# Kernel tuning notes

Hardware: AMD Instinct MI355X
Metric: run time of the kernel (lower is better)

Reference implementation:

```python
import jax, jax.numpy as jnp
import numpy as np

R = 16
ALPHA = 32.0
SCALING = ALPHA / R


def setup_inputs() -> dict:
    key = jax.random.key(0)
    ks = jax.random.split(key, 6)
    B, T, C, O, E = 16, 1500, 1024, 1024, 8
    x = jax.random.normal(ks[0], (B, T, C), dtype=jnp.float32)
    # gate weights per batch element (e.g. softmax-like, but module accepts any)
    w = jax.random.uniform(ks[1], (B, E), dtype=jnp.float32)
    W_base = jax.random.normal(ks[2], (O, C), dtype=jnp.float32) * 0.02
    b_base = jax.random.normal(ks[3], (O,), dtype=jnp.float32) * 0.02
    As = jax.random.normal(ks[4], (E, R, C), dtype=jnp.float32) * 0.02
    Bs = jax.random.normal(ks[5], (E, O, R), dtype=jnp.float32) * 0.02
    return {"x": x, "w": w, "W_base": W_base, "b_base": b_base, "As": As, "Bs": Bs}


def reference(x, w, W_base, b_base, As, Bs):
    # base linear: (B,T,C) @ (C,O) + b
    out = jnp.einsum('btc,oc->bto', x, W_base) + b_base
    # per-expert low-rank: h[b,t,e,r] = x[b,t,:] @ A_e^T
    h = jnp.einsum('btc,erc->bter', x, As)          # (B,T,E,R)
    # y[b,t,e,o] = h @ B_e^T ; gate-weighted sum over experts
    lora = jnp.einsum('bter,eor,be->bto', h, Bs, w)  # (B,T,O)
    return out + lora * SCALING
```

## Files before the change

### kernel.cpp

```cpp
#include <hip/hip_runtime.h>
#include <stdint.h>
#include <stddef.h>


#define B_ 16
#define T_ 1500
#define C_ 1024
#define O_ 1024
#define E_ 8
#define R_ 16
#define ER 128
#define KK 1152
#define BT 24000
#define SCALING 2.0f

typedef __bf16 bf16x8 __attribute__((ext_vector_type(8)));
typedef float f32x4 __attribute__((ext_vector_type(4)));
typedef unsigned short u16;

__device__ inline u16 f2bf(float f) {
  union { float f; unsigned u; } v; v.f = f;
  unsigned u = v.u;
  u += 0x7fff + ((u >> 16) & 1);
  return (u16)(u >> 16);
}

#define GLL(gp, lp)                                                            \
  __builtin_amdgcn_global_load_lds(                                            \
      (const __attribute__((address_space(1))) void*)(gp),                     \
      (__attribute__((address_space(3))) void*)(lp), 16, 0, 0)

__global__ __launch_bounds__(256) void prep_w(const float* __restrict__ Wb,
                                              const float* __restrict__ Bs,
                                              const float* __restrict__ As,
                                              u16* __restrict__ wp,
                                              u16* __restrict__ ap) {
  int idx = blockIdx.x * 256 + threadIdx.x;
  if (idx < O_ * KK) {
    int o = idx / KK;
    int k = idx - o * KK;
    float v;
    if (k < C_) {
      v = Wb[o * C_ + k];
    } else {
      int j = k - C_;
      v = Bs[((j >> 4) * O_ + o) * R_ + (j & 15)];
    }
    wp[idx] = f2bf(v);
  } else {
    int a = idx - O_ * KK;
    ap[a] = f2bf(As[a]);
  }
}

__global__ __launch_bounds__(256) void cvt_h(const float* __restrict__ x,
                                             const u16* __restrict__ ab,
                                             const float* __restrict__ w,
                                             u16* __restrict__ xp) {
  const int mt = blockIdx.x;
  const int tid = threadIdx.x, lane = tid & 63, wv = tid >> 6;
  const int wrow = wv & 1, wcol = wv >> 1, l15 = lane & 15, quad = lane >> 4;
  const int s7 = l15 & 7;

  __shared__ u16 lA[32 * 72];
  __shared__ u16 lB[128 * 64];

  const size_t row0 = (size_t)mt * 32;

  f32x4 acc[4];
#pragma unroll
  for (int j = 0; j < 4; ++j) acc[j] = (f32x4){0.f, 0.f, 0.f, 0.f};

  int brow[4], bko[4];
#pragma unroll
  for (int c = 0; c < 4; ++c) {
    int idx = c * 256 + tid;
    brow[c] = idx >> 3;
    bko[c] = (((idx & 7) ^ (brow[c] & 7)) << 3);
  }

  const int xr = tid >> 3;
  const int xc = (tid & 7) * 4;

  for (int kt = 0; kt < C_ / 64; ++kt) {
    const int k0 = kt * 64;
#pragma unroll
    for (int c = 0; c < 4; ++c)
      GLL(ab + brow[c] * C_ + k0 + bko[c], &lB[(c * 256 + tid) * 8]);
    float4 v0 = *(const float4*)&x[(row0 + xr) * C_ + k0 + xc];
    float4 v1 = *(const float4*)&x[(row0 + xr) * C_ + k0 + 32 + xc];
    ushort4 o0, o1;
    o0.x = f2bf(v0.x); o0.y = f2bf(v0.y); o0.z = f2bf(v0.z); o0.w = f2bf(v0.w);
    o1.x = f2bf(v1.x); o1.y = f2bf(v1.y); o1.z = f2bf(v1.z); o1.w = f2bf(v1.w);
    *(ushort4*)&lA[xr * 72 + xc] = o0;
    *(ushort4*)&lA[xr * 72 + 32 + xc] = o1;
    *(ushort4*)&xp[(row0 + xr) * KK + k0 + xc] = o0;
    *(ushort4*)&xp[(row0 + xr) * KK + k0 + 32 + xc] = o1;
    __syncthreads();
#pragma unroll
    for (int kk = 0; kk < 2; ++kk) {
      bf16x8 af = *(const bf16x8*)&lA[(wrow * 16 + l15) * 72 + kk * 32 + quad * 8];
      bf16x8 bfr[4];
#pragma unroll
      for (int j = 0; j < 4; ++j)
        bfr[j] = *(const bf16x8*)&lB[(wcol * 64 + j * 16 + l15) * 64 +
                                     (((kk * 4 + quad) ^ s7) << 3)];
#pragma unroll
      for (int j = 0; j < 4; ++j)
        acc[j] = __builtin_amdgcn_mfma_f32_16x16x32_bf16(af, bfr[j], acc[j], 0, 0, 0);
    }
    __syncthreads();
  }

#pragma unroll
  for (int j = 0; j < 4; ++j) {
    const int col = wcol * 64 + j * 16 + l15;
    const int e = wcol * 4 + j;
#pragma unroll
    for (int rr = 0; rr < 4; ++rr) {
      const int row = mt * 32 + wrow * 16 + quad * 4 + rr;
      const int b = row / T_;
      xp[(size_t)row * KK + C_ + col] = f2bf(acc[j][rr] * (SCALING * w[b * E_ + e]));
    }
  }
}

__global__ __launch_bounds__(256) void main_gemm(const u16* __restrict__ xp,
                                                 const u16* __restrict__ wp,
                                                 const float* __restrict__ bb,
                                                 float* __restrict__ out) {
  const int id = blockIdx.x;
  const int mt = ((id >> 6) << 3) | (id & 7);
  const int nt = (id >> 3) & 7;
  if (mt >= 188) return;
  const int tid = threadIdx.x, lane = tid & 63, wv = tid >> 6;
  const int wrow = wv & 1, wcol = wv >> 1, l15 = lane & 15, quad = lane >> 4;
  const int s7 = l15 & 7;

  __shared__ u16 lA[128 * 64];
  __shared__ u16 lB[128 * 64];
  const u16* gA = xp + (size_t)mt * 128 * KK;
  const u16* gB = wp + (size_t)nt * 128 * KK;

  f32x4 acc[4][4];
#pragma unroll
  for (int i = 0; i < 4; ++i)
#pragma unroll
    for (int j = 0; j < 4; ++j) acc[i][j] = (f32x4){0.f, 0.f, 0.f, 0.f};

  int srow[4], sko[4];
#pragma unroll
  for (int c = 0; c < 4; ++c) {
    int idx = c * 256 + tid;
    srow[c] = idx >> 3;
    sko[c] = (((idx & 7) ^ (srow[c] & 7)) << 3);
  }

  for (int kt = 0; kt < KK / 64; ++kt) {
    const int k0 = kt * 64;
#pragma unroll
    for (int c = 0; c < 4; ++c)
      GLL(gA + (size_t)srow[c] * KK + k0 + sko[c], &lA[(c * 256 + tid) * 8]);
#pragma unroll
    for (int c = 0; c < 4; ++c)
      GLL(gB + (size_t)srow[c] * KK + k0 + sko[c], &lB[(c * 256 + tid) * 8]);
    __syncthreads();
#pragma unroll
    for (int kk = 0; kk < 2; ++kk) {
      bf16x8 af[4], bfr[4];
#pragma unroll
      for (int i = 0; i < 4; ++i) {
        const int ko = (((kk * 4 + quad) ^ s7) << 3);
        af[i] = *(const bf16x8*)&lA[(wrow * 64 + i * 16 + l15) * 64 + ko];
        bfr[i] = *(const bf16x8*)&lB[(wcol * 64 + i * 16 + l15) * 64 + ko];
      }
#pragma unroll
      for (int i = 0; i < 4; ++i)
#pragma unroll
        for (int j = 0; j < 4; ++j)
          acc[i][j] = __builtin_amdgcn_mfma_f32_16x16x32_bf16(af[i], bfr[j], acc[i][j], 0, 0, 0);
    }
    __syncthreads();
  }

#pragma unroll
  for (int j = 0; j < 4; ++j) {
    const int col = nt * 128 + wcol * 64 + j * 16 + l15;
    const float bias = bb[col];
#pragma unroll
    for (int i = 0; i < 4; ++i) {
#pragma unroll
      for (int rr = 0; rr < 4; ++rr) {
        const int row = mt * 128 + wrow * 64 + i * 16 + quad * 4 + rr;
        if (row < BT) out[(size_t)row * O_ + col] = acc[i][j][rr] + bias;
      }
    }
  }
}

extern "C" void kernel_launch(void* const* d_in, const int* in_sizes, int n_in,
                              void* d_out, int out_size, void* d_ws, size_t ws_size,
                              hipStream_t stream) {
  const float* x = (const float*)d_in[0];
  const float* w = (const float*)d_in[1];
  const float* Wb = (const float*)d_in[2];
  const float* bb = (const float*)d_in[3];
  const float* As = (const float*)d_in[4];
  const float* Bs = (const float*)d_in[5];
  float* out = (float*)d_out;

  u16* xp = (u16*)d_ws;
  u16* wp = xp + (size_t)BT * KK;
  u16* ap = wp + (size_t)O_ * KK;

  prep_w<<<(O_ * KK + ER * C_) / 256, 256, 0, stream>>>(Wb, Bs, As, wp, ap);
  cvt_h<<<750, 256, 0, stream>>>(x, ap, w, xp);
  main_gemm<<<1536, 256, 0, stream>>>(xp, wp, bb, out);
}
```

Before: 285.7 us.

## Double-buffer main GEMM LDS loads with 256x128 tiles and K-step 32

The main GEMM tile grows from 128x128 to 256x128 so each wave holds an 8x4 block of MFMA accumulators, and the K step drops from 64 to 32. LDS is double-buffered and the next tile's global_load_lds is issued before computing on the current one, with explicit waitcnt/barrier control and raised wave priority around the MFMA loop. This aims to overlap global-to-LDS traffic with matrix math and to raise arithmetic intensity per block. In exchange the XOR swizzle is dropped, which may cause LDS bank conflicts, register pressure rises under launch_bounds(256,2), and the grid is halved to 768 blocks (752 active), which increases tail imbalance.

```diff
diff --git a/kernel.cpp b/kernel.cpp
--- a/kernel.cpp
+++ b/kernel.cpp
@@ -12,6 +12,7 @@
 #define ER 128
 #define KK 1152
 #define BT 24000
+#define NT 36
 #define SCALING 2.0f
 
 typedef __bf16 bf16x8 __attribute__((ext_vector_type(8)));
@@ -125,73 +126,97 @@
   }
 }
 
-__global__ __launch_bounds__(256) void main_gemm(const u16* __restrict__ xp,
-                                                 const u16* __restrict__ wp,
-                                                 const float* __restrict__ bb,
-                                                 float* __restrict__ out) {
+__global__ __launch_bounds__(256, 2) void main_gemm(const u16* __restrict__ xp,
+                                                    const u16* __restrict__ wp,
+                                                    const float* __restrict__ bb,
+                                                    float* __restrict__ out) {
   const int id = blockIdx.x;
   const int mt = ((id >> 6) << 3) | (id & 7);
   const int nt = (id >> 3) & 7;
-  if (mt >= 188) return;
+  if (mt >= 94) return;
   const int tid = threadIdx.x, lane = tid & 63, wv = tid >> 6;
-  const int wrow = wv & 1, wcol = wv >> 1, l15 = lane & 15, quad = lane >> 4;
-  const int s7 = l15 & 7;
-
-  __shared__ u16 lA[128 * 64];
-  __shared__ u16 lB[128 * 64];
-  const u16* gA = xp + (size_t)mt * 128 * KK;
+  const int wm = wv >> 1, wn = wv & 1, l15 = lane & 15, quad = lane >> 4;
+
+  __shared__ u16 lA[2][256 * 32];
+  __shared__ u16 lB[2][128 * 32];
+
+  const u16* gA = xp + (size_t)mt * 256 * KK;
   const u16* gB = wp + (size_t)nt * 128 * KK;
 
-  f32x4 acc[4][4];
-#pragma unroll
-  for (int i = 0; i < 4; ++i)
+  f32x4 acc[8][4];
+#pragma unroll
+  for (int i = 0; i < 8; ++i)
 #pragma unroll
     for (int j = 0; j < 4; ++j) acc[i][j] = (f32x4){0.f, 0.f, 0.f, 0.f};
 
-  int srow[4], sko[4];
+  const u16* pa[4];
+  const u16* pb[2];
+  int dA[4], dB[2];
 #pragma unroll
   for (int c = 0; c < 4; ++c) {
     int idx = c * 256 + tid;
-    srow[c] = idx >> 3;
-    sko[c] = (((idx & 7) ^ (srow[c] & 7)) << 3);
-  }
-
-  for (int kt = 0; kt < KK / 64; ++kt) {
-    const int k0 = kt * 64;
-#pragma unroll
-    for (int c = 0; c < 4; ++c)
-      GLL(gA + (size_t)srow[c] * KK + k0 + sko[c], &lA[(c * 256 + tid) * 8]);
-#pragma unroll
-    for (int c = 0; c < 4; ++c)
-      GLL(gB + (size_t)srow[c] * KK + k0 + sko[c], &lB[(c * 256 + tid) * 8]);
-    __syncthreads();
-#pragma unroll
-    for (int kk = 0; kk < 2; ++kk) {
-      bf16x8 af[4], bfr[4];
-#pragma unroll
-      for (int i = 0; i < 4; ++i) {
-        const int ko = (((kk * 4 + quad) ^ s7) << 3);
-        af[i] = *(const bf16x8*)&lA[(wrow * 64 + i * 16 + l15) * 64 + ko];
-        bfr[i] = *(const bf16x8*)&lB[(wcol * 64 + i * 16 + l15) * 64 + ko];
-      }
-#pragma unroll
-      for (int i = 0; i < 4; ++i)
-#pragma unroll
-        for (int j = 0; j < 4; ++j)
-          acc[i][j] = __builtin_amdgcn_mfma_f32_16x16x32_bf16(af[i], bfr[j], acc[i][j], 0, 0, 0);
-    }
-    __syncthreads();
+    pa[c] = gA + (size_t)(idx >> 2) * KK + (idx & 3) * 8;
+    dA[c] = idx * 8;
+  }
+#pragma unroll
+  for (int c = 0; c < 2; ++c) {
+    int idx = c * 256 + tid;
+    pb[c] = gB + (size_t)(idx >> 2) * KK + (idx & 3) * 8;
+    dB[c] = idx * 8;
+  }
+
+  const int offA = (wm * 128 + l15) * 32 + quad * 8;
+  const int offB = (wn * 64 + l15) * 32 + quad * 8;
+
+#pragma unroll
+  for (int c = 0; c < 4; ++c) { GLL(pa[c], &lA[0][dA[c]]); pa[c] += 32; }
+#pragma unroll
+  for (int c = 0; c < 2; ++c) { GLL(pb[c], &lB[0][dB[c]]); pb[c] += 32; }
+
+  for (int t = 0; t < NT; ++t) {
+    const int cur = t & 1, nxt = cur ^ 1;
+    asm volatile("s_waitcnt lgkmcnt(0)" ::: "memory");
+    __builtin_amdgcn_sched_barrier(0);
+    __builtin_amdgcn_s_barrier();
+    __builtin_amdgcn_sched_barrier(0);
+    if (t + 1 < NT) {
+#pragma unroll
+      for (int c = 0; c < 4; ++c) { GLL(pa[c], &lA[nxt][dA[c]]); pa[c] += 32; }
+#pragma unroll
+      for (int c = 0; c < 2; ++c) { GLL(pb[c], &lB[nxt][dB[c]]); pb[c] += 32; }
+      asm volatile("s_waitcnt vmcnt(6)" ::: "memory");
+    } else {
+      asm volatile("s_waitcnt vmcnt(0)" ::: "memory");
+    }
+    __builtin_amdgcn_sched_barrier(0);
+    __builtin_amdgcn_s_barrier();
+    __builtin_amdgcn_sched_barrier(0);
+
+    bf16x8 af[8], bfr[4];
+#pragma unroll
+    for (int i = 0; i < 8; ++i)
+      af[i] = *(const bf16x8*)&lA[cur][offA + i * 512];
+#pragma unroll
+    for (int j = 0; j < 4; ++j)
+      bfr[j] = *(const bf16x8*)&lB[cur][offB + j * 512];
+    __builtin_amdgcn_s_setprio(1);
+#pragma unroll
+    for (int i = 0; i < 8; ++i)
+#pragma unroll
+      for (int j = 0; j < 4; ++j)
+        acc[i][j] = __builtin_amdgcn_mfma_f32_16x16x32_bf16(af[i], bfr[j], acc[i][j], 0, 0, 0);
+    __builtin_amdgcn_s_setprio(0);
   }
 
 #pragma unroll
   for (int j = 0; j < 4; ++j) {
-    const int col = nt * 128 + wcol * 64 + j * 16 + l15;
+    const int col = nt * 128 + wn * 64 + j * 16 + l15;
     const float bias = bb[col];
 #pragma unroll
-    for (int i = 0; i < 4; ++i) {
+    for (int i = 0; i < 8; ++i) {
 #pragma unroll
       for (int rr = 0; rr < 4; ++rr) {
-        const int row = mt * 128 + wrow * 64 + i * 16 + quad * 4 + rr;
+        const int row = mt * 256 + wm * 128 + i * 16 + quad * 4 + rr;
         if (row < BT) out[(size_t)row * O_ + col] = acc[i][j][rr] + bias;
       }
     }
@@ -215,5 +240,5 @@
 
   prep_w<<<(O_ * KK + ER * C_) / 256, 256, 0, stream>>>(Wb, Bs, As, wp, ap);
   cvt_h<<<750, 256, 0, stream>>>(x, ap, w, xp);
-  main_gemm<<<1536, 256, 0, stream>>>(xp, wp, bb, out);
-}
+  main_gemm<<<768, 256, 0, stream>>>(xp, wp, bb, out);
+}
```

Result: slower. 311.8 us (+9.1%).
